# Kernel tuning notes

Hardware: AMD Instinct MI355X
Metric: run time of the kernel (lower is better)

## Reference

```python
import jax, jax.numpy as jnp
import numpy as np

B = 4            # batch (num sequences)
T = 1024         # tokens per sequence (prefill, context_length == tokens_per_seq)
D_MODEL = 4096
H = 32           # n_heads
KVH = 8          # n_kv_heads
HD = D_MODEL // H          # 128
NREP = H // KVH            # 4
BLOCK = 16                 # kv-cache block size
NBLK_PER_SEQ = T // BLOCK  # 64
NBLK = B * NBLK_PER_SEQ    # 256
LAYER_IDX = 0


def _rope(x, positions, cos, sin):
    # x: [N, h, HD]; cos/sin: [max_pos, HD//2]
    c = cos[positions][:, None, :]
    s = sin[positions][:, None, :]
    x1 = x[..., 0::2]
    x2 = x[..., 1::2]
    out = jnp.stack([x1 * c - x2 * s, x1 * s + x2 * c], axis=-1)
    return out.reshape(x.shape)


def setup_inputs() -> dict:
    key = jax.random.key(0)
    ks = jax.random.split(key, 4)
    N = B * T
    x = jax.random.normal(ks[0], (N, D_MODEL), jnp.float32) * 0.02
    w_q = jax.random.normal(ks[1], (D_MODEL, H * HD), jnp.float32) * 0.02
    w_kv = jax.random.normal(ks[2], (D_MODEL, 2 * KVH * HD), jnp.float32) * 0.02
    w_o = jax.random.normal(ks[3], (H * HD, D_MODEL), jnp.float32) * 0.02
    k_cache = jnp.zeros((NBLK, 1, KVH, BLOCK, HD), jnp.float32)
    v_cache = jnp.zeros((NBLK, 1, KVH, BLOCK, HD), jnp.float32)
    # per-token absolute positions: each sequence is a full prefill 0..T-1
    positions = jnp.tile(jnp.arange(T, dtype=jnp.int32), B)          # [N]
    block_tables = jnp.arange(NBLK, dtype=jnp.int32).reshape(B, NBLK_PER_SEQ)
    inv_freq = 1.0 / (10000.0 ** (jnp.arange(0, HD, 2, dtype=jnp.float32) / HD))
    ang = jnp.arange(T, dtype=jnp.float32)[:, None] * inv_freq[None, :]
    rope_cos = jnp.cos(ang)
    rope_sin = jnp.sin(ang)
    return dict(x=x, w_q=w_q, w_kv=w_kv, w_o=w_o, k_cache=k_cache,
                v_cache=v_cache, rope_cos=rope_cos, rope_sin=rope_sin,
                positions=positions, block_tables=block_tables)


def reference(x, w_q, w_kv, w_o, k_cache, v_cache, rope_cos, rope_sin,
              positions, block_tables):
    N = x.shape[0]
    q = (x @ w_q).reshape(N, H, HD)
    k, v = jnp.split(x @ w_kv, 2, axis=-1)
    k = k.reshape(N, KVH, HD)
    v = v.reshape(N, KVH, HD)
    q = _rope(q, positions, rope_cos, rope_sin)
    k = _rope(k, positions, rope_cos, rope_sin)

    # scatter new K/V into the paged cache via block-table indirection
    seq_idx = jnp.repeat(jnp.arange(B), T)                 # [N]
    blk = block_tables[seq_idx, positions // BLOCK]        # [N]
    off = positions % BLOCK                                # [N]
    k_cache = k_cache.at[blk, LAYER_IDX, :, off, :].set(k)
    v_cache = v_cache.at[blk, LAYER_IDX, :, off, :].set(v)

    # gather full context K/V for every sequence from the cache
    kpos = jnp.arange(T, dtype=jnp.int32)
    gblk = block_tables[:, kpos // BLOCK]                  # [B, T]
    goff = (kpos % BLOCK)[None, :]                         # [1, T] -> broadcast
    gk = k_cache[gblk, LAYER_IDX, :, goff, :]              # [B, T, KVH, HD]
    gv = v_cache[gblk, LAYER_IDX, :, goff, :]

    # GQA: repeat kv heads (repeat_interleave over head dim)
    gk = jnp.repeat(gk, NREP, axis=2)                      # [B, T, H, HD]
    gv = jnp.repeat(gv, NREP, axis=2)

    qb = q.reshape(B, T, H, HD)
    scores = jnp.einsum('bqhd,bkhd->bhqk', qb, gk) / jnp.sqrt(jnp.float32(HD))
    qpos = positions.reshape(B, T)
    causal = qpos[:, None, :, None] < kpos[None, None, None, :]  # mask where q < k
    scores = jnp.where(causal, jnp.float32(-1e9), scores)
    probs = jax.nn.softmax(scores.astype(jnp.float32), axis=-1).astype(qb.dtype)
    out = jnp.einsum('bhqk,bkhd->bqhd', probs, gv).reshape(N, H * HD)
    return out @ w_o
```

## Files before the change

kernel.cpp:

```cpp
#include <hip/hip_runtime.h>
#include <hip/hip_bf16.h>


typedef __hip_bfloat16 bf16;
using frag  = __attribute__((ext_vector_type(8))) short;
using facc  = __attribute__((ext_vector_type(4))) float;

static __device__ __forceinline__ bf16 f2b(float x) { return __float2bfloat16(x); }

static __device__ __forceinline__ void async_copy16(const void* g, void* l) {
  __builtin_amdgcn_global_load_lds(
      (const __attribute__((address_space(1))) void*)g,
      (__attribute__((address_space(3))) void*)l, 16, 0, 0);
}

static __device__ __forceinline__ facc mfma16(frag a, frag b, facc c) {
  return __builtin_amdgcn_mfma_f32_16x16x32_bf16(a, b, c, 0, 0, 0);
}

#define SBARRIER() do { __builtin_amdgcn_sched_barrier(0); \
                        __builtin_amdgcn_s_barrier(); \
                        __builtin_amdgcn_sched_barrier(0); } while (0)
#define WAIT_LGKM0() do { asm volatile("s_waitcnt lgkmcnt(0)" ::: "memory"); \
                          __builtin_amdgcn_sched_barrier(0); } while (0)
#define WAIT_VM(n) do { asm volatile("s_waitcnt vmcnt(" #n ")" ::: "memory"); \
                        __builtin_amdgcn_sched_barrier(0); } while (0)


__global__ void convert_x_kernel(const float* __restrict__ in, bf16* __restrict__ out) {
  int i = (blockIdx.x * blockDim.x + threadIdx.x) * 4;
  float4 v = *(const float4*)(in + i);
  out[i + 0] = f2b(v.x);
  out[i + 1] = f2b(v.y);
  out[i + 2] = f2b(v.z);
  out[i + 3] = f2b(v.w);
}

__global__ void transpose_conv_kernel(const float* __restrict__ in, bf16* __restrict__ out,
                                      int rows, int cols) {
  __shared__ float tile[32][33];
  int bx = blockIdx.x * 32;
  int by = blockIdx.y * 32;
  int tx = threadIdx.x, ty = threadIdx.y;
#pragma unroll
  for (int i = 0; i < 32; i += 8)
    tile[ty + i][tx] = in[(size_t)(by + ty + i) * cols + bx + tx];
  __syncthreads();
#pragma unroll
  for (int i = 0; i < 32; i += 8)
    out[(size_t)(bx + ty + i) * rows + by + tx] = f2b(tile[tx][ty + i]);
}


template <int KIND>
static __device__ __forceinline__ void stage_half(const bf16* __restrict__ gsrc,
                                                  char* lds, int Kd, int tid) {
#pragma unroll
  for (int i = 0; i < 2; ++i) {
    int c = i * 512 + tid;
    int chunk;
    if (KIND < 2) chunk = c + ((c >> 9) << 9) + (KIND == 1 ? 512 : 0);
    else          chunk = c + ((c >> 8) << 8) + (KIND == 3 ? 256 : 0);
    int r  = chunk >> 3;
    int gc = (chunk & 7) ^ (r & 7);
    async_copy16(gsrc + (size_t)r * Kd + gc * 8, lds + (size_t)chunk * 16);
  }
}

template <bool OUT_F32>
__global__ __launch_bounds__(512, 2) void gemm256_kernel(
    const bf16* __restrict__ A, const bf16* __restrict__ BT,
    void* __restrict__ Cout, int M, int Nn, int Kd) {
  extern __shared__ char smem[];
  char* As0 = smem;
  char* As1 = smem + 32 * 1024;
  char* Bs0 = smem + 64 * 1024;
  char* Bs1 = smem + 96 * 1024;

  int tid  = threadIdx.x;
  int wave = tid >> 6, lane = tid & 63;
  int ml   = lane & 15, quad = lane >> 4;
  int wm   = wave >> 2, wn = wave & 3;

  int nbx = Nn >> 8;
  int nwg = gridDim.x;
  int id  = blockIdx.x;
  int swz = (id & 7) * (nwg >> 3) + (id >> 3);
  int bm  = (swz / nbx) << 8;
  int bn  = (swz % nbx) << 8;

  const bf16* Ag = A + (size_t)bm * Kd;
  const bf16* Bg = BT + (size_t)bn * Kd;

  facc acc[8][4];
#pragma unroll
  for (int i = 0; i < 8; ++i)
#pragma unroll
    for (int j = 0; j < 4; ++j)
#pragma unroll
      for (int r = 0; r < 4; ++r) acc[i][j][r] = 0.f;

  auto lda = [&](const char* buf, int mh, int mt, int kk) -> frag {
    int row = wm * 128 + mh * 64 + mt * 16 + ml;
    int cs  = (kk * 4 + quad) ^ (ml & 7);
    return *(const frag*)(buf + ((size_t)row * 8 + cs) * 16);
  };
  auto ldb = [&](const char* buf, int nh, int nt, int kk) -> frag {
    int row = wn * 64 + nh * 32 + nt * 16 + ml;
    int cs  = (kk * 4 + quad) ^ (ml & 7);
    return *(const frag*)(buf + ((size_t)row * 8 + cs) * 16);
  };

  int NKT = Kd >> 6;

  stage_half<0>(Ag,      As0, Kd, tid);
  stage_half<2>(Bg,      Bs0, Kd, tid);
  stage_half<1>(Ag,      As0, Kd, tid);
  stage_half<3>(Bg,      Bs0, Kd, tid);
  stage_half<2>(Bg + 64, Bs1, Kd, tid);
  stage_half<0>(Ag + 64, As1, Kd, tid);
  stage_half<3>(Bg + 64, Bs1, Kd, tid);
  WAIT_VM(6);
  SBARRIER();

  frag af[4][2], b0[2][2], b1[2][2];

  for (int kt = 0; kt < NKT; ++kt) {
    const char* Ac = (kt & 1) ? As1 : As0;
    const char* Bc = (kt & 1) ? Bs1 : Bs0;
    char* An = (kt & 1) ? As0 : As1;
    bool s1 = (kt + 1) < NKT;
    bool s2 = (kt + 2) < NKT;
    const bf16* Ag1 = Ag + (size_t)(kt + 1) * 64;
    const bf16* Ag2 = Ag + (size_t)(kt + 2) * 64;
    const bf16* Bg2 = Bg + (size_t)(kt + 2) * 64;

#pragma unroll
    for (int mt = 0; mt < 4; ++mt) {
      af[mt][0] = lda(Ac, 0, mt, 0);
      af[mt][1] = lda(Ac, 0, mt, 1);
    }
#pragma unroll
    for (int nt = 0; nt < 2; ++nt) {
      b0[nt][0] = ldb(Bc, 0, nt, 0);
      b0[nt][1] = ldb(Bc, 0, nt, 1);
    }
    if (s1) stage_half<1>(Ag1, An, Kd, tid);
    SBARRIER(); WAIT_LGKM0();
    __builtin_amdgcn_s_setprio(1);
#pragma unroll
    for (int mt = 0; mt < 4; ++mt)
#pragma unroll
      for (int nt = 0; nt < 2; ++nt) {
        acc[mt][nt] = mfma16(af[mt][0], b0[nt][0], acc[mt][nt]);
        acc[mt][nt] = mfma16(af[mt][1], b0[nt][1], acc[mt][nt]);
      }
    __builtin_amdgcn_s_setprio(0);
    SBARRIER();

#pragma unroll
    for (int nt = 0; nt < 2; ++nt) {
      b1[nt][0] = ldb(Bc, 1, nt, 0);
      b1[nt][1] = ldb(Bc, 1, nt, 1);
    }
    if (s2) stage_half<2>(Bg2, (char*)Bc, Kd, tid);
    SBARRIER(); WAIT_LGKM0();
    __builtin_amdgcn_s_setprio(1);
#pragma unroll
    for (int mt = 0; mt < 4; ++mt)
#pragma unroll
      for (int nt = 0; nt < 2; ++nt) {
        acc[mt][2 + nt] = mfma16(af[mt][0], b1[nt][0], acc[mt][2 + nt]);
        acc[mt][2 + nt] = mfma16(af[mt][1], b1[nt][1], acc[mt][2 + nt]);
      }
    __builtin_amdgcn_s_setprio(0);
    SBARRIER();

#pragma unroll
    for (int mt = 0; mt < 4; ++mt) {
      af[mt][0] = lda(Ac, 1, mt, 0);
      af[mt][1] = lda(Ac, 1, mt, 1);
    }
    if (s2) stage_half<0>(Ag2, (char*)Ac, Kd, tid);
    SBARRIER(); WAIT_LGKM0();
    __builtin_amdgcn_s_setprio(1);
#pragma unroll
    for (int mt = 0; mt < 4; ++mt)
#pragma unroll
      for (int nt = 0; nt < 2; ++nt) {
        acc[4 + mt][2 + nt] = mfma16(af[mt][0], b1[nt][0], acc[4 + mt][2 + nt]);
        acc[4 + mt][2 + nt] = mfma16(af[mt][1], b1[nt][1], acc[4 + mt][2 + nt]);
      }
    __builtin_amdgcn_s_setprio(0);
    SBARRIER();

    if (s2) stage_half<3>(Bg2, (char*)Bc, Kd, tid);
    SBARRIER();
    __builtin_amdgcn_s_setprio(1);
#pragma unroll
    for (int mt = 0; mt < 4; ++mt)
#pragma unroll
      for (int nt = 0; nt < 2; ++nt) {
        acc[4 + mt][nt] = mfma16(af[mt][0], b0[nt][0], acc[4 + mt][nt]);
        acc[4 + mt][nt] = mfma16(af[mt][1], b0[nt][1], acc[4 + mt][nt]);
      }
    __builtin_amdgcn_s_setprio(0);
    if (s2)      { WAIT_VM(6); }
    else if (s1) { WAIT_VM(0); }
    SBARRIER();
  }

#pragma unroll
  for (int mi = 0; mi < 8; ++mi)
#pragma unroll
    for (int ni = 0; ni < 4; ++ni)
#pragma unroll
      for (int r = 0; r < 4; ++r) {
        size_t row = bm + wm * 128 + mi * 16 + quad * 4 + r;
        size_t col = bn + wn * 64 + ni * 16 + ml;
        float v = acc[mi][ni][r];
        if (OUT_F32) ((float*)Cout)[row * Nn + col] = v;
        else         ((bf16*)Cout)[row * Nn + col] = f2b(v);
      }
}


__global__ void rope_kernel(bf16* __restrict__ qh, bf16* __restrict__ kvb,
                            const float* __restrict__ cosb, const float* __restrict__ sinb,
                            const int* __restrict__ positions) {
  const float qscale = 0.08838834764831843f;
  int idx   = blockIdx.x * blockDim.x + threadIdx.x;
  int token = idx / 2560;
  int p     = idx % 2560;
  int pos   = positions[token];
  bf16* base;
  int i;
  float sc;
  if (p < 2048) {
    int hh = p >> 6; i = p & 63;
    base = qh + (size_t)token * 4096 + hh * 128 + 2 * i;
    sc = qscale;
  } else {
    int pk = p - 2048;
    int hh = pk >> 6; i = pk & 63;
    base = kvb + (size_t)token * 2048 + hh * 128 + 2 * i;
    sc = 1.0f;
  }
  float c = cosb[pos * 64 + i] * sc, s = sinb[pos * 64 + i] * sc;
  float x1 = __bfloat162float(base[0]);
  float x2 = __bfloat162float(base[1]);
  base[0] = f2b(x1 * c - x2 * s);
  base[1] = f2b(x1 * s + x2 * c);
}


__global__ void vtrans_kernel(const bf16* __restrict__ kvb, bf16* __restrict__ vt) {
  __shared__ bf16 tile[32][33];
  int dt = blockIdx.x * 32;
  int tt = blockIdx.y * 32;
  int bk = blockIdx.z;
  int b = bk >> 3, kvh = bk & 7;
  const bf16* in = kvb + (size_t)(b * 1024) * 2048 + 1024 + kvh * 128;
  bf16* out = vt + (size_t)bk * 128 * 1024;
  int tx = threadIdx.x, ty = threadIdx.y;
#pragma unroll
  for (int i = 0; i < 32; i += 8)
    tile[ty + i][tx] = in[(size_t)(tt + ty + i) * 2048 + dt + tx];
  __syncthreads();
#pragma unroll
  for (int i = 0; i < 32; i += 8)
    out[(size_t)(dt + ty + i) * 1024 + tt + tx] = tile[tx][ty + i];
}


__global__ __launch_bounds__(512, 4) void attn_kernel(
    const bf16* __restrict__ qh, const bf16* __restrict__ kvb,
    const bf16* __restrict__ vt, bf16* __restrict__ attn) {
  __shared__ alignas(16) bf16 Ks[64 * 128];
  __shared__ alignas(16) bf16 Vs[128 * 64];
  __shared__ alignas(16) bf16 Ps[8][16 * 84];

  int tid  = threadIdx.x;
  int wave = tid >> 6;
  int lane = tid & 63;
  int ml   = lane & 15, quad = lane >> 4;
  int wq   = wave >> 2;
  int wh   = wave & 3;

  int pr  = blockIdx.x;
  int kvh = blockIdx.y;
  int b   = blockIdx.z;
  int h   = kvh * 4 + wh;

  const bf16* kbptr = kvb + (size_t)(b * 1024) * 2048 + kvh * 128;
  const bf16* vbptr = vt + (size_t)((b * 8 + kvh) * 128) * 1024;
  bf16* Pw = &Ps[wave][0];

#pragma unroll
  for (int half = 0; half < 2; ++half) {
    int qtile = half ? pr : (31 - pr);
    int q0 = qtile * 32 + wq * 16;

    frag qf[4];
    const bf16* qrow = qh + (size_t)(b * 1024 + q0 + ml) * 4096 + h * 128;
#pragma unroll
    for (int s = 0; s < 4; ++s) qf[s] = *(const frag*)(qrow + s * 32 + quad * 8);

    facc o[8];
#pragma unroll
    for (int db = 0; db < 8; ++db)
#pragma unroll
      for (int r = 0; r < 4; ++r) o[db][r] = 0.f;
    float m_i[4], l_i[4];
#pragma unroll
    for (int r = 0; r < 4; ++r) { m_i[r] = -1e30f; l_i[r] = 0.f; }

    int nkb = (qtile >> 1) + 1;

    for (int kb = 0; kb < nkb; ++kb) {
      int kbase = kb * 64;
      __syncthreads();
#pragma unroll
      for (int i = 0; i < 2; ++i) {
        int c = i * 512 + tid;
        int row = c >> 4, cs = c & 15;
        int gc = cs ^ (row & 7);
        async_copy16(kbptr + (size_t)(kbase + row) * 2048 + gc * 8, (char*)Ks + c * 16);
      }
#pragma unroll
      for (int i = 0; i < 2; ++i) {
        int c = i * 512 + tid;
        int d = c >> 3, cs = c & 7;
        int gc = cs ^ (d & 7);
        async_copy16(vbptr + (size_t)d * 1024 + kbase + gc * 8, (char*)Vs + c * 16);
      }
      __syncthreads();

      facc sc[4];
#pragma unroll
      for (int kt = 0; kt < 4; ++kt)
#pragma unroll
        for (int r = 0; r < 4; ++r) sc[kt][r] = 0.f;
#pragma unroll
      for (int s = 0; s < 4; ++s)
#pragma unroll
        for (int kt = 0; kt < 4; ++kt) {
          int row = kt * 16 + ml;
          int cs = ((s * 4 + quad) ^ (ml & 7));
          frag kf = *(const frag*)&Ks[row * 128 + cs * 8];
          sc[kt] = __builtin_amdgcn_mfma_f32_16x16x32_bf16(qf[s], kf, sc[kt], 0, 0, 0);
        }

#pragma unroll
      for (int r = 0; r < 4; ++r) {
        int qp = q0 + quad * 4 + r;
        float v[4];
        float mx = -1e30f;
#pragma unroll
        for (int kt = 0; kt < 4; ++kt) {
          float s = sc[kt][r];
          if (qp < kbase + kt * 16 + ml) s = -1e30f;
          v[kt] = s;
          mx = fmaxf(mx, s);
        }
        mx = fmaxf(mx, __shfl_xor(mx, 1));
        mx = fmaxf(mx, __shfl_xor(mx, 2));
        mx = fmaxf(mx, __shfl_xor(mx, 4));
        mx = fmaxf(mx, __shfl_xor(mx, 8));
        float mnew  = fmaxf(m_i[r], mx);
        float alpha = __expf(m_i[r] - mnew);
        m_i[r] = mnew;
        float ps = 0.f;
#pragma unroll
        for (int kt = 0; kt < 4; ++kt) {
          float p = __expf(v[kt] - mnew);
          ps += p;
          Pw[(quad * 4 + r) * 84 + kt * 16 + ml] = f2b(p);
        }
        ps += __shfl_xor(ps, 1);
        ps += __shfl_xor(ps, 2);
        ps += __shfl_xor(ps, 4);
        ps += __shfl_xor(ps, 8);
        l_i[r] = l_i[r] * alpha + ps;
#pragma unroll
        for (int db = 0; db < 8; ++db) o[db][r] *= alpha;
      }
      __syncthreads();

#pragma unroll
      for (int j = 0; j < 2; ++j) {
        frag pf = *(const frag*)&Pw[ml * 84 + j * 32 + quad * 8];
#pragma unroll
        for (int db = 0; db < 8; ++db) {
          int d = db * 16 + ml;
          int cs = ((j * 4 + quad) ^ (ml & 7));
          frag vf = *(const frag*)&Vs[d * 64 + cs * 8];
          o[db] = __builtin_amdgcn_mfma_f32_16x16x32_bf16(pf, vf, o[db], 0, 0, 0);
        }
      }
    }

    bf16* arow = attn + (size_t)(b * 1024 + q0) * 4096 + h * 128;
#pragma unroll
    for (int db = 0; db < 8; ++db)
#pragma unroll
      for (int r = 0; r < 4; ++r) {
        float v = o[db][r] / l_i[r];
        arow[(size_t)(quad * 4 + r) * 4096 + db * 16 + ml] = f2b(v);
      }
  }
}


extern "C" void kernel_launch(void* const* d_in, const int* in_sizes, int n_in,
                              void* d_out, int out_size, void* d_ws, size_t ws_size,
                              hipStream_t stream) {
  const float* x        = (const float*)d_in[0];
  const float* w_q      = (const float*)d_in[1];
  const float* w_kv     = (const float*)d_in[2];
  const float* w_o      = (const float*)d_in[3];
  const float* rope_cos = (const float*)d_in[6];
  const float* rope_sin = (const float*)d_in[7];
  const int*   positions = (const int*)d_in[8];
  float* out = (float*)d_out;

  char* ws = (char*)d_ws;
  const size_t MB = 1024 * 1024;
  bf16* xb    = (bf16*)(ws + 0);
  bf16* wqT   = (bf16*)(ws + 32 * MB);
  bf16* wkvT  = (bf16*)(ws + 64 * MB);
  bf16* woT   = (bf16*)(ws + 80 * MB);
  bf16* qh    = (bf16*)(ws + 112 * MB);
  bf16* kvb   = (bf16*)(ws + 144 * MB);
  bf16* vt    = (bf16*)(ws + 160 * MB);
  bf16* attnb = xb;

  static bool s_attr = false;
  if (!s_attr) {
    hipFuncSetAttribute(reinterpret_cast<const void*>(gemm256_kernel<false>),
                        hipFuncAttributeMaxDynamicSharedMemorySize, 131072);
    hipFuncSetAttribute(reinterpret_cast<const void*>(gemm256_kernel<true>),
                        hipFuncAttributeMaxDynamicSharedMemorySize, 131072);
    s_attr = true;
  }

  convert_x_kernel<<<16384, 256, 0, stream>>>(x, xb);
  transpose_conv_kernel<<<dim3(128, 128), dim3(32, 8), 0, stream>>>(w_q, wqT, 4096, 4096);
  transpose_conv_kernel<<<dim3(64, 128),  dim3(32, 8), 0, stream>>>(w_kv, wkvT, 4096, 2048);
  transpose_conv_kernel<<<dim3(128, 128), dim3(32, 8), 0, stream>>>(w_o, woT, 4096, 4096);

  gemm256_kernel<false><<<dim3(256), 512, 131072, stream>>>(xb, wqT, qh, 4096, 4096, 4096);
  gemm256_kernel<false><<<dim3(128), 512, 131072, stream>>>(xb, wkvT, kvb, 4096, 2048, 4096);

  rope_kernel<<<40960, 256, 0, stream>>>(qh, kvb, rope_cos, rope_sin, positions);
  vtrans_kernel<<<dim3(4, 32, 32), dim3(32, 8), 0, stream>>>(kvb, vt);

  attn_kernel<<<dim3(16, 8, 4), 512, 0, stream>>>(qh, kvb, vt, attnb);

  gemm256_kernel<true><<<dim3(256), 512, 131072, stream>>>(attnb, woT, out, 4096, 4096, 4096);
}
```

Before: 736.8 us.

## Software-pipeline LDS fragment reads ahead of MFMA phases in GEMM mainloop

Restructures the 256x256 GEMM main loop into a two-tile unrolled macro that issues LDS fragment reads for the next phase, and for the next k-tile's first A/B halves, before the current MFMA block. It uses partial lgkmcnt/vmcnt waits instead of full drains. Ping-pong B register buffers let next-tile B fragments load during current compute. This aims to hide LDS read latency and reduce stalls at barriers. The cost is extra register pressure and vmcnt accounting that is fragile, especially for tail tiles where the fixed WAIT_VM(8) may not drain correctly.

```diff
diff --git a/kernel.cpp b/kernel.cpp
--- a/kernel.cpp
+++ b/kernel.cpp
@@ -21,10 +21,13 @@
 #define SBARRIER() do { __builtin_amdgcn_sched_barrier(0); \
                         __builtin_amdgcn_s_barrier(); \
                         __builtin_amdgcn_sched_barrier(0); } while (0)
-#define WAIT_LGKM0() do { asm volatile("s_waitcnt lgkmcnt(0)" ::: "memory"); \
+#define WAIT_LGKM(n) do { asm volatile("s_waitcnt lgkmcnt(" #n ")" ::: "memory"); \
                           __builtin_amdgcn_sched_barrier(0); } while (0)
 #define WAIT_VM(n) do { asm volatile("s_waitcnt vmcnt(" #n ")" ::: "memory"); \
                         __builtin_amdgcn_sched_barrier(0); } while (0)
+#define SCHEDBAR() __builtin_amdgcn_sched_barrier(0)
+#define PRIO1 __builtin_amdgcn_s_setprio(1)
+#define PRIO0 __builtin_amdgcn_s_setprio(0)
 
 
 __global__ void convert_x_kernel(const float* __restrict__ in, bf16* __restrict__ out) {
@@ -66,6 +69,72 @@
     async_copy16(gsrc + (size_t)r * Kd + gc * 8, lds + (size_t)chunk * 16);
   }
 }
+
+#define RDA(DST, BUF, MH)                                         \
+  _Pragma("unroll")                                               \
+  for (int mt = 0; mt < 4; ++mt) {                                \
+    DST[mt][0] = lda(BUF, MH, mt, 0);                             \
+    DST[mt][1] = lda(BUF, MH, mt, 1);                             \
+  }
+
+#define RDB(DST, BUF, NH)                                         \
+  _Pragma("unroll")                                               \
+  for (int nt = 0; nt < 2; ++nt) {                                \
+    DST[nt][0] = ldb(BUF, NH, nt, 0);                             \
+    DST[nt][1] = ldb(BUF, NH, nt, 1);                             \
+  }
+
+#define MFMA_Q(AF, BF, MB, NB)                                    \
+  _Pragma("unroll")                                               \
+  for (int mt = 0; mt < 4; ++mt)                                  \
+    _Pragma("unroll")                                             \
+    for (int nt = 0; nt < 2; ++nt) {                              \
+      acc[(MB) + mt][(NB) + nt] =                                 \
+          mfma16(AF[mt][0], BF[nt][0], acc[(MB) + mt][(NB) + nt]);\
+      acc[(MB) + mt][(NB) + nt] =                                 \
+          mfma16(AF[mt][1], BF[nt][1], acc[(MB) + mt][(NB) + nt]);\
+    }
+
+#define GTILE(AC, BC, AN, BN, B0C, B0N, T)                        \
+  {                                                               \
+    bool s1 = (T) + 1 < NKT;                                      \
+    bool s2 = (T) + 2 < NKT;                                      \
+    const bf16* Ag1 = Ag + (size_t)((T) + 1) * 64;                \
+    const bf16* Ag2 = Ag + (size_t)((T) + 2) * 64;                \
+    const bf16* Bg2 = Bg + (size_t)((T) + 2) * 64;                \
+                                 \
+    if (s1) stage_half<1>(Ag1, AN, Kd, tid);                      \
+    RDB(b1, BC, 1);                                               \
+    SBARRIER();                                                   \
+    WAIT_LGKM(4);                                                 \
+    PRIO1; MFMA_Q(af, B0C, 0, 0); PRIO0;                          \
+    WAIT_VM(8);                                                   \
+    SBARRIER();                                                   \
+                  \
+    if (s2) stage_half<2>(Bg2, (char*)(BC), Kd, tid);             \
+    SBARRIER();                                                   \
+    WAIT_LGKM(0);                                                 \
+    PRIO1; MFMA_Q(af, b1, 0, 2); PRIO0;                           \
+    SCHEDBAR();                                                   \
+    RDA(af, AC, 1);                                               \
+    SBARRIER();                                                   \
+                                 \
+    if (s2) stage_half<0>(Ag2, (char*)(AC), Kd, tid);             \
+    SBARRIER();                                                   \
+    WAIT_LGKM(0);                                                 \
+    PRIO1; MFMA_Q(af, b1, 4, 2); PRIO0;                           \
+    WAIT_VM(8);                                                   \
+    SBARRIER();                                                   \
+    \
+    if (s2) stage_half<3>(Bg2, (char*)(BC), Kd, tid);             \
+    if (s1) { RDB(B0N, BN, 0); }                                  \
+    SBARRIER();                                                   \
+    PRIO1; MFMA_Q(af, B0C, 4, 0); PRIO0;                          \
+    SCHEDBAR();                                                   \
+    if (s1) { RDA(af, AN, 0); }                                   \
+    WAIT_VM(8);                                                   \
+    SBARRIER();                                                   \
+  }
 
 template <bool OUT_F32>
 __global__ __launch_bounds__(512, 2) void gemm256_kernel(
@@ -113,101 +182,26 @@
 
   int NKT = Kd >> 6;
 
+  frag af[4][2], b0e[2][2], b0o[2][2], b1[2][2];
+
+  stage_half<2>(Bg,      Bs0, Kd, tid);
   stage_half<0>(Ag,      As0, Kd, tid);
-  stage_half<2>(Bg,      Bs0, Kd, tid);
+  stage_half<3>(Bg,      Bs0, Kd, tid);
   stage_half<1>(Ag,      As0, Kd, tid);
-  stage_half<3>(Bg,      Bs0, Kd, tid);
   stage_half<2>(Bg + 64, Bs1, Kd, tid);
   stage_half<0>(Ag + 64, As1, Kd, tid);
   stage_half<3>(Bg + 64, Bs1, Kd, tid);
-  WAIT_VM(6);
+  WAIT_VM(10);
   SBARRIER();
-
-  frag af[4][2], b0[2][2], b1[2][2];
-
-  for (int kt = 0; kt < NKT; ++kt) {
-    const char* Ac = (kt & 1) ? As1 : As0;
-    const char* Bc = (kt & 1) ? Bs1 : Bs0;
-    char* An = (kt & 1) ? As0 : As1;
-    bool s1 = (kt + 1) < NKT;
-    bool s2 = (kt + 2) < NKT;
-    const bf16* Ag1 = Ag + (size_t)(kt + 1) * 64;
-    const bf16* Ag2 = Ag + (size_t)(kt + 2) * 64;
-    const bf16* Bg2 = Bg + (size_t)(kt + 2) * 64;
-
-#pragma unroll
-    for (int mt = 0; mt < 4; ++mt) {
-      af[mt][0] = lda(Ac, 0, mt, 0);
-      af[mt][1] = lda(Ac, 0, mt, 1);
-    }
-#pragma unroll
-    for (int nt = 0; nt < 2; ++nt) {
-      b0[nt][0] = ldb(Bc, 0, nt, 0);
-      b0[nt][1] = ldb(Bc, 0, nt, 1);
-    }
-    if (s1) stage_half<1>(Ag1, An, Kd, tid);
-    SBARRIER(); WAIT_LGKM0();
-    __builtin_amdgcn_s_setprio(1);
-#pragma unroll
-    for (int mt = 0; mt < 4; ++mt)
-#pragma unroll
-      for (int nt = 0; nt < 2; ++nt) {
-        acc[mt][nt] = mfma16(af[mt][0], b0[nt][0], acc[mt][nt]);
-        acc[mt][nt] = mfma16(af[mt][1], b0[nt][1], acc[mt][nt]);
-      }
-    __builtin_amdgcn_s_setprio(0);
-    SBARRIER();
-
-#pragma unroll
-    for (int nt = 0; nt < 2; ++nt) {
-      b1[nt][0] = ldb(Bc, 1, nt, 0);
-      b1[nt][1] = ldb(Bc, 1, nt, 1);
-    }
-    if (s2) stage_half<2>(Bg2, (char*)Bc, Kd, tid);
-    SBARRIER(); WAIT_LGKM0();
-    __builtin_amdgcn_s_setprio(1);
-#pragma unroll
-    for (int mt = 0; mt < 4; ++mt)
-#pragma unroll
-      for (int nt = 0; nt < 2; ++nt) {
-        acc[mt][2 + nt] = mfma16(af[mt][0], b1[nt][0], acc[mt][2 + nt]);
-        acc[mt][2 + nt] = mfma16(af[mt][1], b1[nt][1], acc[mt][2 + nt]);
-      }
-    __builtin_amdgcn_s_setprio(0);
-    SBARRIER();
-
-#pragma unroll
-    for (int mt = 0; mt < 4; ++mt) {
-      af[mt][0] = lda(Ac, 1, mt, 0);
-      af[mt][1] = lda(Ac, 1, mt, 1);
-    }
-    if (s2) stage_half<0>(Ag2, (char*)Ac, Kd, tid);
-    SBARRIER(); WAIT_LGKM0();
-    __builtin_amdgcn_s_setprio(1);
-#pragma unroll
-    for (int mt = 0; mt < 4; ++mt)
-#pragma unroll
-      for (int nt = 0; nt < 2; ++nt) {
-        acc[4 + mt][2 + nt] = mfma16(af[mt][0], b1[nt][0], acc[4 + mt][2 + nt]);
-        acc[4 + mt][2 + nt] = mfma16(af[mt][1], b1[nt][1], acc[4 + mt][2 + nt]);
-      }
-    __builtin_amdgcn_s_setprio(0);
-    SBARRIER();
-
-    if (s2) stage_half<3>(Bg2, (char*)Bc, Kd, tid);
-    SBARRIER();
-    __builtin_amdgcn_s_setprio(1);
-#pragma unroll
-    for (int mt = 0; mt < 4; ++mt)
-#pragma unroll
-      for (int nt = 0; nt < 2; ++nt) {
-        acc[4 + mt][nt] = mfma16(af[mt][0], b0[nt][0], acc[4 + mt][nt]);
-        acc[4 + mt][nt] = mfma16(af[mt][1], b0[nt][1], acc[4 + mt][nt]);
-      }
-    __builtin_amdgcn_s_setprio(0);
-    if (s2)      { WAIT_VM(6); }
-    else if (s1) { WAIT_VM(0); }
-    SBARRIER();
+  RDB(b0e, Bs0, 0);
+  SCHEDBAR();
+  RDA(af, As0, 0);
+  WAIT_VM(8);
+  SBARRIER();
+
+  for (int kt = 0; kt < NKT; kt += 2) {
+    GTILE(As0, Bs0, As1, Bs1, b0e, b0o, kt);
+    GTILE(As1, Bs1, As0, Bs0, b0o, b0e, kt + 1);
   }
 
 #pragma unroll
```

Result: faster. 708.5 us (-3.8%).
